# Performance work log

Hardware: AMD Instinct MI355X
Metric: run time of the kernel (lower is better)

The kernel has to match this reference:

```python
import jax, jax.numpy as jnp
import numpy as np

B, CIN, H, W = 256, 1280, 7, 7
A, NCLS, HID, NGT = 9, 20, 128, 40
OUT_DIM = 5 * A + NCLS  # 65


def setup_inputs() -> dict:
    key = jax.random.key(0)
    ks = jax.random.split(key, 8)
    features = jax.random.normal(ks[0], (B, CIN, H, W), jnp.float32)
    # grid: (x, y) centers of each feature cell, in feature-map coordinates
    grid = jax.random.uniform(ks[1], (B, H, W, 2), jnp.float32) * 7.0
    # GT boxes (x1, y1, x2, y2, class), padded count NGT per image
    xy1 = jax.random.uniform(ks[2], (B, NGT, 2), jnp.float32) * 5.0
    wh = jax.random.uniform(ks[3], (B, NGT, 2), jnp.float32) * 2.0 + 0.5
    cls = jax.random.randint(ks[4], (B, NGT, 1), 0, NCLS).astype(jnp.float32)
    bboxes = jnp.concatenate([xy1, xy1 + wh, cls], axis=-1)
    # anchor shapes (w, h) as in SingleStageDetector.__init__
    anc = jnp.array([[1.0, 1], [2, 2], [3, 3], [4, 4], [5, 5],
                     [2, 3], [3, 2], [3, 5], [5, 3]], jnp.float32)
    W1 = jax.random.normal(ks[5], (HID, CIN), jnp.float32) * 0.02
    b1 = jnp.zeros((HID,), jnp.float32)
    W2 = jax.random.normal(ks[6], (OUT_DIM, HID), jnp.float32) * 0.02
    b2 = jnp.zeros((OUT_DIM,), jnp.float32)
    return dict(features=features, grid=grid, bboxes=bboxes, anc=anc,
                W1=W1, b1=b1, W2=W2, b2=b2)


def reference(features, grid, bboxes, anc, W1, b1, W2, b2):
    Bx = features.shape[0]
    # --- PredictionNetwork (inference mode; dropout is identity at eval) ---
    h = jnp.einsum('bchw,oc->bohw', features, W1) + b1[None, :, None, None]
    h = jax.nn.leaky_relu(h, negative_slope=0.01)
    out = jnp.einsum('bchw,oc->bohw', h, W2) + b2[None, :, None, None]
    conf_scores = jax.nn.sigmoid(out[:, 4 * A:5 * A])          # (B, A, H, W)
    offsets = out[:, :4 * A].reshape(Bx, A, 4, H, W)
    offsets = jnp.concatenate(
        [jax.nn.sigmoid(offsets[:, :, :2]) - 0.5, offsets[:, :, 2:]], axis=2)
    class_scores = out[:, 5 * A:]                               # (B, C, H, W)
    # --- GenerateAnchor: (B, A, H, W, 4) as (x_tl, y_tl, x_br, y_br) ---
    ctr = grid[:, None]                    # (B, 1, H, W, 2)
    half = anc[None, :, None, None, :] / 2  # (1, A, 1, 1, 2)
    anchors = jnp.concatenate([ctr - half, ctr + half], axis=-1)
    # --- IoU: (B, A*H*W, N) ---
    P = anchors.reshape(Bx, -1, 4)          # (B, AHW, 4)
    gt = bboxes[..., :4]                    # (B, N, 4)
    tl = jnp.maximum(P[:, :, None, :2], gt[:, None, :, :2])
    br = jnp.minimum(P[:, :, None, 2:], gt[:, None, :, 2:])
    inter = jnp.prod(jnp.clip(br - tl, 0.0), axis=-1)  # (B, AHW, N)
    # torch code zeroes intersections for proposals with any coord <= 0
    legal = (jnp.min(P, axis=-1) > 0)[..., None]
    inter = inter * legal
    p_area = ((P[:, :, 2] - P[:, :, 0]) * (P[:, :, 3] - P[:, :, 1]))[:, :, None]
    g_area = ((gt[:, :, 2] - gt[:, :, 0]) * (gt[:, :, 3] - gt[:, :, 1]))[:, None, :]
    iou_mat = inter / (g_area + p_area - inter)
    return (conf_scores, offsets, class_scores, iou_mat)
```

## Files before the change

kernel.cpp:

```cpp
#include <hip/hip_runtime.h>


#define CIN_  1280
#define HW_   49
#define HID_  128
#define OUTD_ 65
#define NGT_  40
#define NP_   441

#define CONF_OFF 0
#define OFFS_OFF 112896
#define CLS_OFF  564480
#define IOU_OFF  815360

#define WS_W1F_U32 81920u
#define WS_W2F_U32 5120u

typedef __bf16 bf16x8 __attribute__((ext_vector_type(8)));
typedef float  f32x4  __attribute__((ext_vector_type(4)));

__device__ __forceinline__ unsigned pack2bf(float lo, float hi) {
    unsigned a = __float_as_uint(lo);
    unsigned b = __float_as_uint(hi);
    a = (a + 0x7FFFu + ((a >> 16) & 1u)) >> 16;
    b = (b + 0x7FFFu + ((b >> 16) & 1u)) >> 16;
    return a | (b << 16);
}
__device__ __forceinline__ float sigmoidf_(float v) { return 1.f / (1.f + __expf(-v)); }

__device__ __forceinline__ bf16x8 ld_frag(const unsigned* p) {
    union { uint4 u; bf16x8 v; } x;
    x.u = *(const uint4*)p;
    return x.v;
}
__device__ __forceinline__ bf16x8 as_bf(uint4 u) {
    union { uint4 u; bf16x8 v; } x; x.u = u; return x.v;
}

__global__ __launch_bounds__(256) void prep_w(
    const float* __restrict__ W1, const float* __restrict__ W2,
    unsigned* __restrict__ ws)
{
    int X = blockIdx.x * 256 + threadIdx.x;
    if (X < (int)WS_W1F_U32) {
        int sub = X & 3, lane = (X >> 2) & 63, f = X >> 8;
        int mt = f & 7, K32 = f >> 3;
        int o = mt * 16 + (lane & 15);
        int c = K32 * 32 + (lane >> 4) * 8 + sub * 2;
        float2 v = *(const float2*)(W1 + o * CIN_ + c);
        ws[X] = pack2bf(v.x, v.y);
    } else {
        int Y = X - (int)WS_W1F_U32;
        int sub = Y & 3, lane = (Y >> 2) & 63, f = Y >> 8;
        int mt2 = f % 5, ks2 = f / 5;
        int o2 = mt2 * 16 + (lane & 15);
        int c = ks2 * 32 + (lane >> 4) * 8 + sub * 2;
        unsigned val = 0;
        if (o2 < OUTD_) {
            float2 v = *(const float2*)(W2 + o2 * HID_ + c);
            val = pack2bf(v.x, v.y);
        }
        ws[WS_W1F_U32 + Y] = val;
    }
}

__global__ __launch_bounds__(512, 4) void fused_main(
    const float* __restrict__ F,
    const float* __restrict__ grd,
    const float* __restrict__ bbox,
    const float* __restrict__ anc,
    const unsigned* __restrict__ wsW,
    const float* __restrict__ B1,
    const float* __restrict__ B2,
    float* __restrict__ out)
{
    __shared__ __align__(16) unsigned lds[32 * 640];
    unsigned* smHT = lds;

    const int tid  = threadIdx.x;
    const int b    = blockIdx.x >> 1;
    const int half = blockIdx.x & 1;
    const int lane = tid & 63;
    const int w    = tid >> 6;
    const int quad = lane >> 4;
    const int m16  = lane & 15;
    const int hw0  = half * 32;

    const float* Fb = F + b * (CIN_ * HW_);

    #pragma unroll
    for (int g = 0; g < 5; ++g) {
        float f0[8], f1[8];
        #pragma unroll
        for (int u = 0; u < 8; ++u) {
            int i   = (g * 8 + u) * 512 + tid;
            int cp  = i >> 5;
            int row = i & 31;
            int hw  = hw0 + row;
            bool ok = hw < HW_;
            f0[u] = ok ? Fb[(2 * cp) * HW_ + hw] : 0.f;
            f1[u] = ok ? Fb[(2 * cp + 1) * HW_ + hw] : 0.f;
        }
        #pragma unroll
        for (int u = 0; u < 8; ++u) {
            int i   = (g * 8 + u) * 512 + tid;
            int cp  = i >> 5;
            int row = i & 31;
            int cb = cp >> 2, sub = cp & 3;
            lds[row * 640 + ((cb ^ (row & 7)) << 2) + sub] = pack2bf(f0[u], f1[u]);
        }
    }
    __syncthreads();

    const uint4* Ap = (const uint4*)wsW + w * 64 + lane;
    const unsigned* r0b = lds + m16 * 640;
    const unsigned* r1b = lds + (16 + m16) * 640;
    const int swz = (m16 & 7);

    f32x4 acc0 = (f32x4)(0.f), acc1 = (f32x4)(0.f);
    uint4 a0 = Ap[0];
    uint4 a1 = Ap[512];
    for (int k = 0; k < 40; ++k) {
        uint4 an;
        if (k < 38) an = Ap[(k + 2) * 512];
        int off = ((k * 4 + quad) ^ swz) << 2;
        bf16x8 A = as_bf(a0);
        bf16x8 b0 = ld_frag(r0b + off);
        bf16x8 b1 = ld_frag(r1b + off);
        acc0 = __builtin_amdgcn_mfma_f32_16x16x32_bf16(A, b0, acc0, 0, 0, 0);
        acc1 = __builtin_amdgcn_mfma_f32_16x16x32_bf16(A, b1, acc1, 0, 0, 0);
        a0 = a1; a1 = an;
    }

    const int m2a = w % 5, nt2a = w / 5;
    const uint4* A2p = (const uint4*)(wsW + WS_W1F_U32) + m2a * 64 + lane;
    uint4 a20 = A2p[0], a21 = A2p[320], a22 = A2p[640], a23 = A2p[960];

    __syncthreads();

    #pragma unroll
    for (int nt = 0; nt < 2; ++nt) {
        f32x4 ac = nt ? acc1 : acc0;
        int r0 = nt * 16 + m16;
        #pragma unroll
        for (int rp = 0; rp < 2; ++rp) {
            int o0 = w * 16 + quad * 4 + 2 * rp;
            float v0 = ac[2 * rp]     + B1[o0];
            float v1 = ac[2 * rp + 1] + B1[o0 + 1];
            v0 = v0 > 0.f ? v0 : 0.01f * v0;
            v1 = v1 > 0.f ? v1 : 0.01f * v1;
            smHT[r0 * 68 + (o0 >> 1)] = pack2bf(v0, v1);
        }
    }
    __syncthreads();

    {
        f32x4 c2 = (f32x4)(0.f);
        const unsigned* Bb = smHT + (nt2a * 16 + m16) * 68 + quad * 4;
        c2 = __builtin_amdgcn_mfma_f32_16x16x32_bf16(as_bf(a20), ld_frag(Bb +  0), c2, 0, 0, 0);
        c2 = __builtin_amdgcn_mfma_f32_16x16x32_bf16(as_bf(a21), ld_frag(Bb + 16), c2, 0, 0, 0);
        c2 = __builtin_amdgcn_mfma_f32_16x16x32_bf16(as_bf(a22), ld_frag(Bb + 32), c2, 0, 0, 0);
        c2 = __builtin_amdgcn_mfma_f32_16x16x32_bf16(as_bf(a23), ld_frag(Bb + 48), c2, 0, 0, 0);
        int hw = hw0 + nt2a * 16 + m16;
        if (hw < HW_) {
            #pragma unroll
            for (int r = 0; r < 4; ++r) {
                int o2 = m2a * 16 + quad * 4 + r;
                if (o2 >= OUTD_) continue;
                float aa = c2[r] + B2[o2];
                unsigned dst; float val;
                if (o2 < 36) {
                    int an9 = o2 >> 2, kk = o2 & 3;
                    val = (kk < 2) ? (sigmoidf_(aa) - 0.5f) : aa;
                    dst = OFFS_OFF + b * 1764 + an9 * 196 + kk * 49 + hw;
                } else if (o2 < 45) {
                    val = sigmoidf_(aa);
                    dst = CONF_OFF + b * 441 + (o2 - 36) * 49 + hw;
                } else {
                    val = aa;
                    dst = CLS_OFF + b * 980 + (o2 - 45) * 49 + hw;
                }
                out[dst] = val;
            }
        }
    }
    if (w < 2) {
        const int m2b = 3 + w;
        const uint4* A3p = (const uint4*)(wsW + WS_W1F_U32) + m2b * 64 + lane;
        uint4 b20 = A3p[0], b21 = A3p[320], b22 = A3p[640], b23 = A3p[960];
        f32x4 c2 = (f32x4)(0.f);
        const unsigned* Bb = smHT + (16 + m16) * 68 + quad * 4;
        c2 = __builtin_amdgcn_mfma_f32_16x16x32_bf16(as_bf(b20), ld_frag(Bb +  0), c2, 0, 0, 0);
        c2 = __builtin_amdgcn_mfma_f32_16x16x32_bf16(as_bf(b21), ld_frag(Bb + 16), c2, 0, 0, 0);
        c2 = __builtin_amdgcn_mfma_f32_16x16x32_bf16(as_bf(b22), ld_frag(Bb + 32), c2, 0, 0, 0);
        c2 = __builtin_amdgcn_mfma_f32_16x16x32_bf16(as_bf(b23), ld_frag(Bb + 48), c2, 0, 0, 0);
        int hw = hw0 + 16 + m16;
        if (hw < HW_) {
            #pragma unroll
            for (int r = 0; r < 4; ++r) {
                int o2 = m2b * 16 + quad * 4 + r;
                if (o2 >= OUTD_) continue;
                float aa = c2[r] + B2[o2];
                unsigned dst; float val;
                if (o2 < 36) {
                    int an9 = o2 >> 2, kk = o2 & 3;
                    val = (kk < 2) ? (sigmoidf_(aa) - 0.5f) : aa;
                    dst = OFFS_OFF + b * 1764 + an9 * 196 + kk * 49 + hw;
                } else if (o2 < 45) {
                    val = sigmoidf_(aa);
                    dst = CONF_OFF + b * 441 + (o2 - 36) * 49 + hw;
                } else {
                    val = aa;
                    dst = CLS_OFF + b * 980 + (o2 - 45) * 49 + hw;
                }
                out[dst] = val;
            }
        }
    }

    {
        int gl = (lane < NGT_) ? lane : 0;
        const float* gb = bbox + b * 200 + gl * 5;
        float gx1 = gb[0], gy1 = gb[1], gx2 = gb[2], gy2 = gb[3];
        float gA = (gx2 - gx1) * (gy2 - gy1);
        const int pstart = half ? 221 : 0;
        const int pend   = half ? NP_ : 221;
        #pragma unroll 4
        for (int p = pstart + w; p < pend; p += 8) {
            int a9 = p / 49, r = p - a9 * 49;
            float2 ct = *(const float2*)(grd + b * 98 + 2 * r);
            float hx = anc[2 * a9] * 0.5f,  hy = anc[2 * a9 + 1] * 0.5f;
            float px1 = ct.x - hx, py1 = ct.y - hy, px2 = ct.x + hx, py2 = ct.y + hy;
            float pA = (px2 - px1) * (py2 - py1);
            float legal = (fminf(fminf(px1, py1), fminf(px2, py2)) > 0.f) ? 1.f : 0.f;
            float tlx = fmaxf(px1, gx1), tly = fmaxf(py1, gy1);
            float brx = fminf(px2, gx2), bry = fminf(py2, gy2);
            float dx = fmaxf(brx - tlx, 0.f), dy = fmaxf(bry - tly, 0.f);
            float inter = dx * dy * legal;
            float iou = inter / (gA + pA - inter);
            if (lane < NGT_)
                out[IOU_OFF + b * (NP_ * NGT_) + p * 40 + lane] = iou;
        }
    }
}

extern "C" void kernel_launch(void* const* d_in, const int* in_sizes, int n_in,
                              void* d_out, int out_size, void* d_ws, size_t ws_size,
                              hipStream_t stream) {
    const float* F  = (const float*)d_in[0];
    const float* G  = (const float*)d_in[1];
    const float* BB = (const float*)d_in[2];
    const float* AN = (const float*)d_in[3];
    const float* W1 = (const float*)d_in[4];
    const float* B1 = (const float*)d_in[5];
    const float* W2 = (const float*)d_in[6];
    const float* B2 = (const float*)d_in[7];
    float* out = (float*)d_out;
    unsigned* wsu = (unsigned*)d_ws;

    prep_w<<<340, 256, 0, stream>>>(W1, W2, wsu);
    fused_main<<<512, 512, 0, stream>>>(F, G, BB, AN, wsu, B1, B2, out);
}
```

Measured before the change: 133.5 us.

## Split each image into four 16-pixel blocks to double grid size

Each image's spatial tile now goes to four blocks of 16 pixels each, up from two blocks of 32. That doubles the grid to 1024 blocks and halves the LDS footprint, so launch bounds now allow 8 blocks per CU. Each block runs one MFMA chain in the first layer instead of two, and the second-layer work is handled by five waves. In exchange, every block re-reads all of W1 from global/L2, doubling weight traffic, and the last quarter block holds only one valid pixel.

Result: slower. 145.6 us (+9.1%).

```diff
diff --git a/kernel.cpp b/kernel.cpp
--- a/kernel.cpp
+++ b/kernel.cpp
@@ -64,7 +64,7 @@
     }
 }
 
-__global__ __launch_bounds__(512, 4) void fused_main(
+__global__ __launch_bounds__(512, 8) void fused_main(
     const float* __restrict__ F,
     const float* __restrict__ grd,
     const float* __restrict__ bbox,
@@ -74,38 +74,38 @@
     const float* __restrict__ B2,
     float* __restrict__ out)
 {
-    __shared__ __align__(16) unsigned lds[32 * 640];
+    __shared__ __align__(16) unsigned lds[16 * 640];
     unsigned* smHT = lds;
 
     const int tid  = threadIdx.x;
-    const int b    = blockIdx.x >> 1;
-    const int half = blockIdx.x & 1;
+    const int b    = blockIdx.x >> 2;
+    const int qtr  = blockIdx.x & 3;
     const int lane = tid & 63;
     const int w    = tid >> 6;
     const int quad = lane >> 4;
     const int m16  = lane & 15;
-    const int hw0  = half * 32;
+    const int hw0  = qtr * 16;
 
     const float* Fb = F + b * (CIN_ * HW_);
 
     #pragma unroll
-    for (int g = 0; g < 5; ++g) {
-        float f0[8], f1[8];
+    for (int g = 0; g < 4; ++g) {
+        float f0[5], f1[5];
         #pragma unroll
-        for (int u = 0; u < 8; ++u) {
-            int i   = (g * 8 + u) * 512 + tid;
-            int cp  = i >> 5;
-            int row = i & 31;
+        for (int u = 0; u < 5; ++u) {
+            int i   = (g * 5 + u) * 512 + tid;
+            int cp  = i >> 4;
+            int row = i & 15;
             int hw  = hw0 + row;
             bool ok = hw < HW_;
             f0[u] = ok ? Fb[(2 * cp) * HW_ + hw] : 0.f;
             f1[u] = ok ? Fb[(2 * cp + 1) * HW_ + hw] : 0.f;
         }
         #pragma unroll
-        for (int u = 0; u < 8; ++u) {
-            int i   = (g * 8 + u) * 512 + tid;
-            int cp  = i >> 5;
-            int row = i & 31;
+        for (int u = 0; u < 5; ++u) {
+            int i   = (g * 5 + u) * 512 + tid;
+            int cp  = i >> 4;
+            int row = i & 15;
             int cb = cp >> 2, sub = cp & 3;
             lds[row * 640 + ((cb ^ (row & 7)) << 2) + sub] = pack2bf(f0[u], f1[u]);
         }
@@ -114,58 +114,50 @@
 
     const uint4* Ap = (const uint4*)wsW + w * 64 + lane;
     const unsigned* r0b = lds + m16 * 640;
-    const unsigned* r1b = lds + (16 + m16) * 640;
     const int swz = (m16 & 7);
 
-    f32x4 acc0 = (f32x4)(0.f), acc1 = (f32x4)(0.f);
+    f32x4 acc0 = (f32x4)(0.f);
     uint4 a0 = Ap[0];
     uint4 a1 = Ap[512];
     for (int k = 0; k < 40; ++k) {
         uint4 an;
         if (k < 38) an = Ap[(k + 2) * 512];
         int off = ((k * 4 + quad) ^ swz) << 2;
-        bf16x8 A = as_bf(a0);
-        bf16x8 b0 = ld_frag(r0b + off);
-        bf16x8 b1 = ld_frag(r1b + off);
-        acc0 = __builtin_amdgcn_mfma_f32_16x16x32_bf16(A, b0, acc0, 0, 0, 0);
-        acc1 = __builtin_amdgcn_mfma_f32_16x16x32_bf16(A, b1, acc1, 0, 0, 0);
+        acc0 = __builtin_amdgcn_mfma_f32_16x16x32_bf16(as_bf(a0), ld_frag(r0b + off), acc0, 0, 0, 0);
         a0 = a1; a1 = an;
     }
 
-    const int m2a = w % 5, nt2a = w / 5;
-    const uint4* A2p = (const uint4*)(wsW + WS_W1F_U32) + m2a * 64 + lane;
-    uint4 a20 = A2p[0], a21 = A2p[320], a22 = A2p[640], a23 = A2p[960];
+    uint4 a20 = {}, a21 = {}, a22 = {}, a23 = {};
+    if (w < 5) {
+        const uint4* A2p = (const uint4*)(wsW + WS_W1F_U32) + w * 64 + lane;
+        a20 = A2p[0]; a21 = A2p[320]; a22 = A2p[640]; a23 = A2p[960];
+    }
 
     __syncthreads();
 
     #pragma unroll
-    for (int nt = 0; nt < 2; ++nt) {
-        f32x4 ac = nt ? acc1 : acc0;
-        int r0 = nt * 16 + m16;
-        #pragma unroll
-        for (int rp = 0; rp < 2; ++rp) {
-            int o0 = w * 16 + quad * 4 + 2 * rp;
-            float v0 = ac[2 * rp]     + B1[o0];
-            float v1 = ac[2 * rp + 1] + B1[o0 + 1];
-            v0 = v0 > 0.f ? v0 : 0.01f * v0;
-            v1 = v1 > 0.f ? v1 : 0.01f * v1;
-            smHT[r0 * 68 + (o0 >> 1)] = pack2bf(v0, v1);
-        }
+    for (int rp = 0; rp < 2; ++rp) {
+        int o0 = w * 16 + quad * 4 + 2 * rp;
+        float v0 = acc0[2 * rp]     + B1[o0];
+        float v1 = acc0[2 * rp + 1] + B1[o0 + 1];
+        v0 = v0 > 0.f ? v0 : 0.01f * v0;
+        v1 = v1 > 0.f ? v1 : 0.01f * v1;
+        smHT[m16 * 68 + (o0 >> 1)] = pack2bf(v0, v1);
     }
     __syncthreads();
 
-    {
+    if (w < 5) {
         f32x4 c2 = (f32x4)(0.f);
-        const unsigned* Bb = smHT + (nt2a * 16 + m16) * 68 + quad * 4;
+        const unsigned* Bb = smHT + m16 * 68 + quad * 4;
         c2 = __builtin_amdgcn_mfma_f32_16x16x32_bf16(as_bf(a20), ld_frag(Bb +  0), c2, 0, 0, 0);
         c2 = __builtin_amdgcn_mfma_f32_16x16x32_bf16(as_bf(a21), ld_frag(Bb + 16), c2, 0, 0, 0);
         c2 = __builtin_amdgcn_mfma_f32_16x16x32_bf16(as_bf(a22), ld_frag(Bb + 32), c2, 0, 0, 0);
         c2 = __builtin_amdgcn_mfma_f32_16x16x32_bf16(as_bf(a23), ld_frag(Bb + 48), c2, 0, 0, 0);
-        int hw = hw0 + nt2a * 16 + m16;
+        int hw = hw0 + m16;
         if (hw < HW_) {
             #pragma unroll
             for (int r = 0; r < 4; ++r) {
-                int o2 = m2a * 16 + quad * 4 + r;
+                int o2 = w * 16 + quad * 4 + r;
                 if (o2 >= OUTD_) continue;
                 float aa = c2[r] + B2[o2];
                 unsigned dst; float val;
@@ -184,47 +176,14 @@
             }
         }
     }
-    if (w < 2) {
-        const int m2b = 3 + w;
-        const uint4* A3p = (const uint4*)(wsW + WS_W1F_U32) + m2b * 64 + lane;
-        uint4 b20 = A3p[0], b21 = A3p[320], b22 = A3p[640], b23 = A3p[960];
-        f32x4 c2 = (f32x4)(0.f);
-        const unsigned* Bb = smHT + (16 + m16) * 68 + quad * 4;
-        c2 = __builtin_amdgcn_mfma_f32_16x16x32_bf16(as_bf(b20), ld_frag(Bb +  0), c2, 0, 0, 0);
-        c2 = __builtin_amdgcn_mfma_f32_16x16x32_bf16(as_bf(b21), ld_frag(Bb + 16), c2, 0, 0, 0);
-        c2 = __builtin_amdgcn_mfma_f32_16x16x32_bf16(as_bf(b22), ld_frag(Bb + 32), c2, 0, 0, 0);
-        c2 = __builtin_amdgcn_mfma_f32_16x16x32_bf16(as_bf(b23), ld_frag(Bb + 48), c2, 0, 0, 0);
-        int hw = hw0 + 16 + m16;
-        if (hw < HW_) {
-            #pragma unroll
-            for (int r = 0; r < 4; ++r) {
-                int o2 = m2b * 16 + quad * 4 + r;
-                if (o2 >= OUTD_) continue;
-                float aa = c2[r] + B2[o2];
-                unsigned dst; float val;
-                if (o2 < 36) {
-                    int an9 = o2 >> 2, kk = o2 & 3;
-                    val = (kk < 2) ? (sigmoidf_(aa) - 0.5f) : aa;
-                    dst = OFFS_OFF + b * 1764 + an9 * 196 + kk * 49 + hw;
-                } else if (o2 < 45) {
-                    val = sigmoidf_(aa);
-                    dst = CONF_OFF + b * 441 + (o2 - 36) * 49 + hw;
-                } else {
-                    val = aa;
-                    dst = CLS_OFF + b * 980 + (o2 - 45) * 49 + hw;
-                }
-                out[dst] = val;
-            }
-        }
-    }
 
     {
         int gl = (lane < NGT_) ? lane : 0;
         const float* gb = bbox + b * 200 + gl * 5;
         float gx1 = gb[0], gy1 = gb[1], gx2 = gb[2], gy2 = gb[3];
         float gA = (gx2 - gx1) * (gy2 - gy1);
-        const int pstart = half ? 221 : 0;
-        const int pend   = half ? NP_ : 221;
+        const int pstart = (qtr * NP_) >> 2;
+        const int pend   = ((qtr + 1) * NP_) >> 2;
         #pragma unroll 4
         for (int p = pstart + w; p < pend; p += 8) {
             int a9 = p / 49, r = p - a9 * 49;
@@ -259,5 +218,5 @@
     unsigned* wsu = (unsigned*)d_ws;
 
     prep_w<<<340, 256, 0, stream>>>(W1, W2, wsu);
-    fused_main<<<512, 512, 0, stream>>>(F, G, BB, AN, wsu, B1, B2, out);
-}
+    fused_main<<<1024, 512, 0, stream>>>(F, G, BB, AN, wsu, B1, B2, out);
+}
```

## Double-buffer feature staging in LDS to overlap global loads with MFMA

Applied to the files above, without the earlier changes.

Instead of staging all 1280 channels of the feature tile into LDS before the GEMM, the kernel now stages 256-channel chunks into a double-buffered LDS region. Global loads for the next chunk are issued before the MFMA loop over the current chunk, and the packed result is written after it, so memory latency can hide behind compute. The LDS footprint drops from 80KB to 32KB, which may allow more resident blocks, at the cost of five extra barriers and more live registers for the in-flight loads. Stores also become 16-byte vector writes.

After: 135.6 us. Within noise of the previous version (+1.6%).

```diff
diff --git a/kernel.cpp b/kernel.cpp
--- a/kernel.cpp
+++ b/kernel.cpp
@@ -74,7 +74,7 @@
     const float* __restrict__ B2,
     float* __restrict__ out)
 {
-    __shared__ __align__(16) unsigned lds[32 * 640];
+    __shared__ __align__(16) unsigned lds[2 * 32 * 128];
     unsigned* smHT = lds;
 
     const int tid  = threadIdx.x;
@@ -88,55 +88,73 @@
 
     const float* Fb = F + b * (CIN_ * HW_);
 
-    #pragma unroll
-    for (int g = 0; g < 5; ++g) {
-        float f0[8], f1[8];
-        #pragma unroll
-        for (int u = 0; u < 8; ++u) {
-            int i   = (g * 8 + u) * 512 + tid;
-            int cp  = i >> 5;
-            int row = i & 31;
-            int hw  = hw0 + row;
-            bool ok = hw < HW_;
-            f0[u] = ok ? Fb[(2 * cp) * HW_ + hw] : 0.f;
-            f1[u] = ok ? Fb[(2 * cp + 1) * HW_ + hw] : 0.f;
-        }
-        #pragma unroll
-        for (int u = 0; u < 8; ++u) {
-            int i   = (g * 8 + u) * 512 + tid;
-            int cp  = i >> 5;
-            int row = i & 31;
-            int cb = cp >> 2, sub = cp & 3;
-            lds[row * 640 + ((cb ^ (row & 7)) << 2) + sub] = pack2bf(f0[u], f1[u]);
-        }
-    }
-    __syncthreads();
-
+    const int srow = tid & 31;
+    const int shw  = hw0 + srow;
+    const bool sok = shw < HW_;
+    const int cb0  = (tid >> 5) * 2;
+    const float* Fs = Fb + shw;
+
+    float fl[16];
+    #define STAGE_ISSUE(c)                                                   \
+        {                                                                    \
+            _Pragma("unroll")                                                \
+            for (int u = 0; u < 2; ++u) {                                    \
+                _Pragma("unroll")                                            \
+                for (int j = 0; j < 8; ++j) {                                \
+                    int ch = (c) * 256 + (cb0 + u) * 8 + j;                  \
+                    fl[u * 8 + j] = sok ? Fs[ch * HW_] : 0.f;                \
+                }                                                            \
+            }                                                                \
+        }
+    #define STAGE_WRITE(c)                                                   \
+        {                                                                    \
+            unsigned* dstb = lds + (((c) & 1) << 12) + srow * 128;           \
+            _Pragma("unroll")                                                \
+            for (int u = 0; u < 2; ++u) {                                    \
+                int cb = cb0 + u;                                            \
+                uint4 q;                                                     \
+                q.x = pack2bf(fl[u * 8 + 0], fl[u * 8 + 1]);                 \
+                q.y = pack2bf(fl[u * 8 + 2], fl[u * 8 + 3]);                 \
+                q.z = pack2bf(fl[u * 8 + 4], fl[u * 8 + 5]);                 \
+                q.w = pack2bf(fl[u * 8 + 6], fl[u * 8 + 7]);                 \
+                *(uint4*)(dstb + ((cb ^ (srow & 7)) << 2)) = q;              \
+            }                                                                \
+        }
+
+    STAGE_ISSUE(0);
     const uint4* Ap = (const uint4*)wsW + w * 64 + lane;
-    const unsigned* r0b = lds + m16 * 640;
-    const unsigned* r1b = lds + (16 + m16) * 640;
-    const int swz = (m16 & 7);
-
-    f32x4 acc0 = (f32x4)(0.f), acc1 = (f32x4)(0.f);
     uint4 a0 = Ap[0];
     uint4 a1 = Ap[512];
-    for (int k = 0; k < 40; ++k) {
-        uint4 an;
-        if (k < 38) an = Ap[(k + 2) * 512];
-        int off = ((k * 4 + quad) ^ swz) << 2;
-        bf16x8 A = as_bf(a0);
-        bf16x8 b0 = ld_frag(r0b + off);
-        bf16x8 b1 = ld_frag(r1b + off);
-        acc0 = __builtin_amdgcn_mfma_f32_16x16x32_bf16(A, b0, acc0, 0, 0, 0);
-        acc1 = __builtin_amdgcn_mfma_f32_16x16x32_bf16(A, b1, acc1, 0, 0, 0);
-        a0 = a1; a1 = an;
+    STAGE_WRITE(0);
+    __syncthreads();
+
+    const unsigned* r0base = lds + m16 * 128;
+    const unsigned* r1base = lds + (16 + m16) * 128;
+    const int swz = (m16 & 7);
+
+    f32x4 acc0 = (f32x4)(0.f), acc1 = (f32x4)(0.f);
+    int kglob = 0;
+    #pragma unroll
+    for (int c = 0; c < 5; ++c) {
+        if (c < 4) STAGE_ISSUE(c + 1);
+        const int boff = (c & 1) << 12;
+        #pragma unroll
+        for (int kk = 0; kk < 8; ++kk) {
+            int kp = kglob + 2; if (kp > 39) kp = 39;
+            uint4 an = Ap[kp * 512];
+            int off = (((kk << 2) + quad) ^ swz) << 2;
+            bf16x8 A = as_bf(a0);
+            acc0 = __builtin_amdgcn_mfma_f32_16x16x32_bf16(A, ld_frag(r0base + boff + off), acc0, 0, 0, 0);
+            acc1 = __builtin_amdgcn_mfma_f32_16x16x32_bf16(A, ld_frag(r1base + boff + off), acc1, 0, 0, 0);
+            a0 = a1; a1 = an; ++kglob;
+        }
+        if (c < 4) STAGE_WRITE(c + 1);
+        __syncthreads();
     }
 
     const int m2a = w % 5, nt2a = w / 5;
     const uint4* A2p = (const uint4*)(wsW + WS_W1F_U32) + m2a * 64 + lane;
     uint4 a20 = A2p[0], a21 = A2p[320], a22 = A2p[640], a23 = A2p[960];
-
-    __syncthreads();
 
     #pragma unroll
     for (int nt = 0; nt < 2; ++nt) {
```
